# Performance work log

Hardware: AMD Instinct MI355X
Metric: run time of the kernel (lower is better)

## Reference

```python
import jax, jax.numpy as jnp
import numpy as np

N_NODES = 100000
N_EDGES = 1600000  # total after symmetrization (800k pairs + reverses)
N_GRAPHS = 64
D_IN = 64
D_HID = 128
N_CLASSES = 10


def setup_inputs() -> dict:
    key = jax.random.key(0)
    ks = jax.random.split(key, 16)
    half = N_EDGES // 2
    src = jax.random.randint(ks[0], (half,), 0, N_NODES)
    dst = jax.random.randint(ks[1], (half,), 0, N_NODES)
    dst = jnp.where(dst == src, (dst + 1) % N_NODES, dst)  # no self-loops
    # to_undirected: symmetric edge list with fixed shape [2, E]
    edge_index = jnp.stack([jnp.concatenate([src, dst]),
                            jnp.concatenate([dst, src])]).astype(jnp.int64)
    # sorted balanced graph assignment: every graph id present
    batch = ((jnp.arange(N_NODES) * N_GRAPHS) // N_NODES).astype(jnp.int64)

    def lin(k, fi, fo):
        return jax.random.normal(k, (fi, fo), jnp.float32) * (1.0 / np.sqrt(fi))

    inp = {
        'x': jax.random.normal(ks[2], (N_NODES, D_IN), jnp.float32),
        'edge_index': edge_index,
        'batch': batch,
        'gin1_w1': lin(ks[3], D_IN, D_HID), 'gin1_b1': jnp.zeros((D_HID,), jnp.float32),
        'gin1_w2': lin(ks[4], D_HID, D_HID), 'gin1_b2': jnp.zeros((D_HID,), jnp.float32),
        'gin2_w1': lin(ks[5], D_HID, D_HID), 'gin2_b1': jnp.zeros((D_HID,), jnp.float32),
        'gin2_w2': lin(ks[6], D_HID, D_HID), 'gin2_b2': jnp.zeros((D_HID,), jnp.float32),
        'gin3_w1': lin(ks[7], D_HID, D_HID), 'gin3_b1': jnp.zeros((D_HID,), jnp.float32),
        'gin3_w2': lin(ks[8], D_HID, D_HID), 'gin3_b2': jnp.zeros((D_HID,), jnp.float32),
        'fc1_w': lin(ks[9], D_HID, 64), 'fc1_b': jnp.zeros((64,), jnp.float32),
        'fc2_w': lin(ks[10], 64, N_CLASSES), 'fc2_b': jnp.zeros((N_CLASSES,), jnp.float32),
    }
    return inp


def _gin_layer(x, src, dst, w1, b1, w2, b2):
    # GINConv (eps=0): h_i = MLP(x_i + sum_{j in N(i)} x_j)
    agg = jax.ops.segment_sum(x[src], dst, num_segments=N_NODES)
    h = x + agg
    h = jax.nn.relu(h @ w1 + b1)
    return h @ w2 + b2


def reference(x, edge_index, batch,
              gin1_w1, gin1_b1, gin1_w2, gin1_b2,
              gin2_w1, gin2_b1, gin2_w2, gin2_b2,
              gin3_w1, gin3_b1, gin3_w2, gin3_b2,
              fc1_w, fc1_b, fc2_w, fc2_b):
    src, dst = edge_index[0], edge_index[1]
    h = _gin_layer(x, src, dst, gin1_w1, gin1_b1, gin1_w2, gin1_b2)
    h = _gin_layer(h, src, dst, gin2_w1, gin2_b1, gin2_w2, gin2_b2)
    h = _gin_layer(h, src, dst, gin3_w1, gin3_b1, gin3_w2, gin3_b2)
    # global_max_pool over graphs
    pooled = jax.ops.segment_max(h, batch, num_segments=N_GRAPHS)  # [G, D_HID]
    out = jax.nn.relu(pooled @ fc1_w + fc1_b) @ fc2_w + fc2_b
    return jax.nn.log_softmax(out, axis=1)
```

## Files before the change

kernel.cpp:

```cpp
#include <hip/hip_runtime.h>
#include <hip/hip_bf16.h>
#include <cmath>

#define NNODES 100000
#define NGRAPHS 64
#define SHIFT 9
#define NPB 512
#define NB 196
#define CAP 12288
#define BIN_CHUNK 4096
#define HSTRIDE 136
#define CONVBLK 6250

typedef __attribute__((ext_vector_type(8))) short bf16x8;
typedef __attribute__((ext_vector_type(4))) float f32x4;
typedef __attribute__((ext_vector_type(4))) unsigned int u32x4;

__device__ __forceinline__ float bf2f(unsigned short u) {
    unsigned int v = ((unsigned int)u) << 16;
    return __uint_as_float(v);
}
__device__ __forceinline__ unsigned short f2bf(float f) {
    unsigned int v = __float_as_uint(f);
    unsigned int r = (v + 0x7fffu + ((v >> 16) & 1u)) >> 16;
    return (unsigned short)r;
}

__device__ __forceinline__ void atomicMaxF(float* addr, float v) {
    if (v >= 0.f) atomicMax((int*)addr, __float_as_int(v));
    else          atomicMin((unsigned int*)addr, __float_as_uint(v));
}

__device__ __forceinline__ void pack_one(unsigned short* wp, const float* W, int K, int t) {
    int total = (K / 32) * 8 * 64;
    if (t >= total) return;
    int l = t & 63;
    int n0 = (t >> 6) & 7;
    int kp = t >> 9;
    unsigned short o[8];
#pragma unroll
    for (int j = 0; j < 8; ++j)
        o[j] = f2bf(W[(size_t)(kp * 32 + (l >> 4) * 8 + j) * 128 + n0 * 16 + (l & 15)]);
    *(u32x4*)(wp + (size_t)t * 8) = *(u32x4*)o;
}

__global__ __launch_bounds__(256) void setup_kernel(
        unsigned short* __restrict__ B0, const float* __restrict__ x,
        unsigned short* wp1, const float* g1w1,
        unsigned short* wp2, const float* g1w2,
        unsigned short* wp3, const float* g2w1,
        unsigned short* wp4, const float* g2w2,
        unsigned short* wp5, const float* g3w1,
        unsigned short* wp6, const float* g3w2,
        float* __restrict__ pooled, int* __restrict__ gcur) {
    int b = blockIdx.x;
    int t = threadIdx.x;
    if (b < CONVBLK) {
        int i = b * 256 + t;
        float4 v = ((const float4*)x)[i];
        unsigned short o[4] = { f2bf(v.x), f2bf(v.y), f2bf(v.z), f2bf(v.w) };
        ((uint2*)B0)[i] = *(uint2*)o;
        return;
    }
    b -= CONVBLK;
    if (b < 44) {
        if (b < 4)       pack_one(wp1, g1w1, 64,  b * 256 + t);
        else if (b < 12) pack_one(wp2, g1w2, 128, (b - 4) * 256 + t);
        else if (b < 20) pack_one(wp3, g2w1, 128, (b - 12) * 256 + t);
        else if (b < 28) pack_one(wp4, g2w2, 128, (b - 20) * 256 + t);
        else if (b < 36) pack_one(wp5, g3w1, 128, (b - 28) * 256 + t);
        else             pack_one(wp6, g3w2, 128, (b - 36) * 256 + t);
        return;
    }
    b -= 44;
    if (b < 32) {
        pooled[b * 256 + t] = -INFINITY;
        return;
    }
    if (t < NB) gcur[t] = t * CAP;
}

__global__ __launch_bounds__(256) void bin_kernel(unsigned int* __restrict__ binned,
                                                  int* __restrict__ gcur,
                                                  const int* __restrict__ ei, int E) {
    __shared__ int cnt[NB];
    __shared__ int gbase[NB];
    __shared__ int loff[NB];
    int t = threadIdx.x;
    int base = blockIdx.x * BIN_CHUNK;
    for (int i = t; i < NB; i += 256) { cnt[i] = 0; loff[i] = 0; }
    __syncthreads();
    unsigned int pk[16]; short bk[16]; int ne = 0;
#pragma unroll
    for (int i = 0; i < 16; ++i) {
        int e = base + t + i * 256;
        if (e < E) {
            int s = ei[e], d = ei[E + e];
            int b = d >> SHIFT;
            pk[ne] = ((unsigned int)s << SHIFT) | (unsigned int)(d & (NPB - 1));
            bk[ne] = (short)b;
            ne++;
            atomicAdd(&cnt[b], 1);
        }
    }
    __syncthreads();
    for (int i = t; i < NB; i += 256)
        gbase[i] = cnt[i] ? atomicAdd(&gcur[i], cnt[i]) : 0;
    __syncthreads();
    for (int i = 0; i < ne; ++i) {
        int b = bk[i];
        int pos = atomicAdd(&loff[b], 1);
        binned[gbase[b] + pos] = pk[i];
    }
}

__global__ __launch_bounds__(256) void fill2_kernel(int* __restrict__ csr,
                                                    int* __restrict__ start,
                                                    const unsigned int* __restrict__ binned,
                                                    const int* __restrict__ gcur, int N) {
    __shared__ int cur[NPB];
    __shared__ int tsum[256];
    __shared__ int gbs[2];
    int b = blockIdx.x, t = threadIdx.x;
    int n0 = b << SHIFT;
    int nn = N - n0; if (nn > NPB) nn = NPB;
    int c = gcur[b] - b * CAP;
    if (t == 0) {
        int acc = 0, tot = 0;
        for (int i = 0; i < NB; ++i) {
            int ci = gcur[i] - i * CAP;
            if (i < b) acc += ci;
            tot += ci;
        }
        gbs[0] = acc; gbs[1] = tot;
    }
    const unsigned int* eb = binned + (size_t)b * CAP;
    for (int i = t; i < NPB; i += 256) cur[i] = 0;
    __syncthreads();
    int gb = gbs[0];
    for (int p = t; p < c; p += 256) atomicAdd(&cur[eb[p] & (NPB - 1)], 1);
    __syncthreads();
    int v[2]; int s = 0;
#pragma unroll
    for (int i = 0; i < 2; ++i) { v[i] = cur[t * 2 + i]; s += v[i]; }
    int x = s;
    tsum[t] = x;
    __syncthreads();
    for (int off = 1; off < 256; off <<= 1) {
        int y = (t >= off) ? tsum[t - off] : 0;
        __syncthreads();
        x += y;
        tsum[t] = x;
        __syncthreads();
    }
    int run = x - s + gb;
#pragma unroll
    for (int i = 0; i < 2; ++i) {
        int idx = t * 2 + i;
        cur[idx] = run;
        if (idx < nn) start[n0 + idx] = run;
        run += v[i];
    }
    __syncthreads();
    for (int p = t; p < c; p += 256) {
        unsigned int e = eb[p];
        int slot = atomicAdd(&cur[e & (NPB - 1)], 1);
        csr[slot] = (int)(e >> SHIFT);
    }
    if (t == 0 && b == 0) start[N] = gbs[1];
}

template<int K1, bool POOL>
__global__ __launch_bounds__(256) void fused_layer(const unsigned short* __restrict__ Hin,
                                                   const int* __restrict__ start,
                                                   const int* __restrict__ csr,
                                                   const unsigned short* __restrict__ Wp1,
                                                   const float* __restrict__ bias1,
                                                   const unsigned short* __restrict__ Wp2,
                                                   const float* __restrict__ bias2,
                                                   unsigned short* __restrict__ out,
                                                   const int* __restrict__ batch,
                                                   float* __restrict__ pooled, int M) {
    __shared__ unsigned short tile[64 * HSTRIDE];
    __shared__ unsigned int lmax[2][128];
    const int l = threadIdx.x & 63;
    const int w = threadIdx.x >> 6;
    const int rbase = blockIdx.x * 64 + w * 16;
    unsigned short* wt = tile + (w * 16) * HSTRIDE;

    if (POOL) {
        ((unsigned int*)lmax)[threadIdx.x] = 0x007fffffu;
        __syncthreads();
    }

    constexpr int LANES = (K1 == 128) ? 16 : 8;
    constexpr int RPP = 64 / LANES;
    const int rg = l / LANES;
    const int ch = l % LANES;
    const unsigned short* hbb = Hin + ch * 8;
#pragma unroll
    for (int pass = 0; pass < 16 / RPP; ++pass) {
        int rloc = pass * RPP + rg;
        int row = rbase + rloc;
        int rowc = row < M ? row : M - 1;
        float a0[8], a1[8];
        {
            u32x4 v = *(const u32x4*)(hbb + (size_t)rowc * K1);
            const unsigned short* q = (const unsigned short*)&v;
#pragma unroll
            for (int i = 0; i < 8; ++i) { a0[i] = bf2f(q[i]); a1[i] = 0.f; }
        }
        int p0 = start[rowc], p1 = start[rowc + 1];
        int p = p0;
        for (; p + 4 <= p1; p += 4) {
            int j0 = csr[p], j1 = csr[p + 1], j2 = csr[p + 2], j3 = csr[p + 3];
            u32x4 v0 = *(const u32x4*)(hbb + (size_t)j0 * K1);
            u32x4 v1 = *(const u32x4*)(hbb + (size_t)j1 * K1);
            u32x4 v2 = *(const u32x4*)(hbb + (size_t)j2 * K1);
            u32x4 v3 = *(const u32x4*)(hbb + (size_t)j3 * K1);
            const unsigned short* q0 = (const unsigned short*)&v0;
            const unsigned short* q1 = (const unsigned short*)&v1;
            const unsigned short* q2 = (const unsigned short*)&v2;
            const unsigned short* q3 = (const unsigned short*)&v3;
#pragma unroll
            for (int i = 0; i < 8; ++i) a0[i] += bf2f(q0[i]);
#pragma unroll
            for (int i = 0; i < 8; ++i) a1[i] += bf2f(q1[i]);
#pragma unroll
            for (int i = 0; i < 8; ++i) a0[i] += bf2f(q2[i]);
#pragma unroll
            for (int i = 0; i < 8; ++i) a1[i] += bf2f(q3[i]);
        }
        for (; p < p1; ++p) {
            int j = csr[p];
            u32x4 v = *(const u32x4*)(hbb + (size_t)j * K1);
            const unsigned short* q = (const unsigned short*)&v;
#pragma unroll
            for (int i = 0; i < 8; ++i) a0[i] += bf2f(q[i]);
        }
        unsigned short o[8];
#pragma unroll
        for (int i = 0; i < 8; ++i) o[i] = f2bf(a0[i] + a1[i]);
        *(u32x4*)(wt + rloc * HSTRIDE + ch * 8) = *(u32x4*)o;
    }

    const int kgrp = l >> 4;
    const int col = l & 15;
    f32x4 acc[8];
#pragma unroll
    for (int i = 0; i < 8; ++i) acc[i] = (f32x4){0.f, 0.f, 0.f, 0.f};
#pragma unroll
    for (int kp = 0; kp < K1 / 32; ++kp) {
        bf16x8 a = *(const bf16x8*)(wt + col * HSTRIDE + kp * 32 + kgrp * 8);
#pragma unroll
        for (int n0 = 0; n0 < 8; ++n0) {
            bf16x8 bfr = *(const bf16x8*)(Wp1 + ((size_t)(kp * 8 + n0) * 64 + l) * 8);
            acc[n0] = __builtin_amdgcn_mfma_f32_16x16x32_bf16(a, bfr, acc[n0], 0, 0, 0);
        }
    }

#pragma unroll
    for (int n0 = 0; n0 < 8; ++n0) {
        float bv = bias1[n0 * 16 + col];
#pragma unroll
        for (int r = 0; r < 4; ++r) {
            float v = acc[n0][r] + bv;
            v = fmaxf(v, 0.f);
            wt[(kgrp * 4 + r) * HSTRIDE + n0 * 16 + col] = f2bf(v);
        }
    }

    f32x4 acc2[8];
#pragma unroll
    for (int i = 0; i < 8; ++i) acc2[i] = (f32x4){0.f, 0.f, 0.f, 0.f};
#pragma unroll
    for (int kp = 0; kp < 4; ++kp) {
        bf16x8 a2 = *(const bf16x8*)(wt + col * HSTRIDE + kp * 32 + kgrp * 8);
#pragma unroll
        for (int n0 = 0; n0 < 8; ++n0) {
            bf16x8 bfr = *(const bf16x8*)(Wp2 + ((size_t)(kp * 8 + n0) * 64 + l) * 8);
            acc2[n0] = __builtin_amdgcn_mfma_f32_16x16x32_bf16(a2, bfr, acc2[n0], 0, 0, 0);
        }
    }

    const int mbase = rbase;
    if (POOL) {
        int g0 = batch[blockIdx.x * 64];
        int gi[4]; bool ok[4];
#pragma unroll
        for (int r = 0; r < 4; ++r) {
            int row = mbase + kgrp * 4 + r;
            ok[r] = (row < M);
            gi[r] = ok[r] ? (batch[row] - g0) : 0;
        }
#pragma unroll
        for (int n0 = 0; n0 < 8; ++n0) {
            int f = n0 * 16 + col;
            float bv = bias2[f];
#pragma unroll
            for (int r = 0; r < 4; ++r) {
                if (ok[r]) {
                    float v = acc2[n0][r] + bv;
                    unsigned int u = __float_as_uint(v);
                    unsigned int key = (u & 0x80000000u) ? ~u : (u | 0x80000000u);
                    atomicMax(&lmax[gi[r]][f], key);
                }
            }
        }
        __syncthreads();
        int t = threadIdx.x;
        unsigned int key = ((unsigned int*)lmax)[t];
        unsigned int u2 = (key & 0x80000000u) ? (key & 0x7fffffffu) : ~key;
        float v = __uint_as_float(u2);
        int g = g0 + (t >> 7);
        if (g < NGRAPHS && key != 0x007fffffu)
            atomicMaxF(&pooled[g * 128 + (t & 127)], v);
    } else {
#pragma unroll
        for (int n0 = 0; n0 < 8; ++n0) {
            float bv = bias2[n0 * 16 + col];
#pragma unroll
            for (int r = 0; r < 4; ++r) {
                int row = mbase + kgrp * 4 + r;
                if (row < M)
                    out[(size_t)row * 128 + n0 * 16 + col] = f2bf(acc2[n0][r] + bv);
            }
        }
    }
}

__global__ __launch_bounds__(64) void head_kernel(float* __restrict__ out,
                                                  const float* __restrict__ pooled,
                                                  const float* __restrict__ w1,
                                                  const float* __restrict__ b1,
                                                  const float* __restrict__ w2,
                                                  const float* __restrict__ b2) {
    int g = blockIdx.x, t = threadIdx.x;
    __shared__ float a[64];
    __shared__ float o[10];
    __shared__ float red[2];
    const float* pg = pooled + g * 128;
    float acc = b1[t];
    for (int k = 0; k < 128; ++k) acc = fmaf(pg[k], w1[k * 64 + t], acc);
    a[t] = fmaxf(acc, 0.f);
    __syncthreads();
    if (t < 10) {
        float s = b2[t];
        for (int k = 0; k < 64; ++k) s = fmaf(a[k], w2[k * 10 + t], s);
        o[t] = s;
    }
    __syncthreads();
    if (t == 0) {
        float m = -INFINITY;
        for (int c = 0; c < 10; ++c) m = fmaxf(m, o[c]);
        float se = 0.f;
        for (int c = 0; c < 10; ++c) se += expf(o[c] - m);
        red[0] = m;
        red[1] = logf(se);
    }
    __syncthreads();
    if (t < 10) out[g * 10 + t] = o[t] - red[0] - red[1];
}

extern "C" void kernel_launch(void* const* d_in, const int* in_sizes, int n_in,
                              void* d_out, int out_size, void* d_ws, size_t ws_size,
                              hipStream_t stream) {
    const float* x    = (const float*)d_in[0];
    const int* ei     = (const int*)d_in[1];
    const int* batch  = (const int*)d_in[2];
    const float* g1w1 = (const float*)d_in[3];  const float* g1b1 = (const float*)d_in[4];
    const float* g1w2 = (const float*)d_in[5];  const float* g1b2 = (const float*)d_in[6];
    const float* g2w1 = (const float*)d_in[7];  const float* g2b1 = (const float*)d_in[8];
    const float* g2w2 = (const float*)d_in[9];  const float* g2b2 = (const float*)d_in[10];
    const float* g3w1 = (const float*)d_in[11]; const float* g3b1 = (const float*)d_in[12];
    const float* g3w2 = (const float*)d_in[13]; const float* g3b2 = (const float*)d_in[14];
    const float* f1w  = (const float*)d_in[15]; const float* f1b  = (const float*)d_in[16];
    const float* f2w  = (const float*)d_in[17]; const float* f2b  = (const float*)d_in[18];
    float* out = (float*)d_out;

    const int N = NNODES;
    const int E = in_sizes[1] / 2;

    char* base = (char*)d_ws;
    auto alloc = [&](size_t bytes) { char* p = base; base += (bytes + 255) & ~(size_t)255; return p; };

    char* shared_region = alloc((size_t)N * 128 * 2);
    unsigned short* B1 = (unsigned short*)shared_region;
    unsigned int* binned = (unsigned int*)shared_region;
    unsigned short* B2 = (unsigned short*)alloc((size_t)N * 128 * 2);
    unsigned short* B0 = (unsigned short*)alloc((size_t)N * 64 * 2);
    int* csr      = (int*)alloc((size_t)E * 4);
    int* start    = (int*)alloc((size_t)(N + 1) * 4);
    int* gcur     = (int*)alloc((size_t)(NB + 4) * 4);
    float* pooled = (float*)alloc((size_t)NGRAPHS * 128 * 4);
    unsigned short* wp1 = (unsigned short*)alloc((size_t)64 * 128 * 2);
    unsigned short* wp2 = (unsigned short*)alloc((size_t)128 * 128 * 2);
    unsigned short* wp3 = (unsigned short*)alloc((size_t)128 * 128 * 2);
    unsigned short* wp4 = (unsigned short*)alloc((size_t)128 * 128 * 2);
    unsigned short* wp5 = (unsigned short*)alloc((size_t)128 * 128 * 2);
    unsigned short* wp6 = (unsigned short*)alloc((size_t)128 * 128 * 2);

    setup_kernel<<<CONVBLK + 44 + 32 + 1, 256, 0, stream>>>(
        B0, x, wp1, g1w1, wp2, g1w2, wp3, g2w1, wp4, g2w2, wp5, g3w1, wp6, g3w2,
        pooled, gcur);
    bin_kernel<<<(E + BIN_CHUNK - 1) / BIN_CHUNK, 256, 0, stream>>>(binned, gcur, ei, E);
    fill2_kernel<<<NB, 256, 0, stream>>>(csr, start, binned, gcur, N);

    const int pgrid = (N + 63) / 64;

    fused_layer<64, false><<<pgrid, 256, 0, stream>>>(B0, start, csr, wp1, g1b1, wp2, g1b2, B1, batch, pooled, N);
    fused_layer<128, false><<<pgrid, 256, 0, stream>>>(B1, start, csr, wp3, g2b1, wp4, g2b2, B2, batch, pooled, N);
    fused_layer<128, true><<<pgrid, 256, 0, stream>>>(B2, start, csr, wp5, g3b1, wp6, g3b2, (unsigned short*)nullptr, batch, pooled, N);

    head_kernel<<<NGRAPHS, 64, 0, stream>>>(out, pooled, f1w, f1b, f2w, f2b);
}
```

Baseline: 284.3 us.

## Halve rows per block and split MLP output columns across wave pairs

Each block now handles 32 rows instead of 64. Each wave gathers 8 rows. For the two MFMA GEMMs, pairs of waves share a 16-row tile and each wave computes half of the 128 output columns, so per-wave accumulator count and B-fragment loads are halved. Twice as many blocks are launched, and block-wide barriers are added between the gather, GEMM1, ReLU write-back and GEMM2 stages. The aims are more parallelism and occupancy with fewer registers per wave, at the cost of extra __syncthreads and more pooling atomics across the larger grid.

```diff
diff --git a/kernel.cpp b/kernel.cpp
--- a/kernel.cpp
+++ b/kernel.cpp
@@ -181,16 +181,14 @@
                                                    unsigned short* __restrict__ out,
                                                    const int* __restrict__ batch,
                                                    float* __restrict__ pooled, int M) {
-    __shared__ unsigned short tile[64 * HSTRIDE];
+    __shared__ unsigned short tile[32 * HSTRIDE];
     __shared__ unsigned int lmax[2][128];
     const int l = threadIdx.x & 63;
     const int w = threadIdx.x >> 6;
-    const int rbase = blockIdx.x * 64 + w * 16;
-    unsigned short* wt = tile + (w * 16) * HSTRIDE;
+    const int rbase = blockIdx.x * 32;
 
     if (POOL) {
         ((unsigned int*)lmax)[threadIdx.x] = 0x007fffffu;
-        __syncthreads();
     }
 
     constexpr int LANES = (K1 == 128) ? 16 : 8;
@@ -199,8 +197,8 @@
     const int ch = l % LANES;
     const unsigned short* hbb = Hin + ch * 8;
 #pragma unroll
-    for (int pass = 0; pass < 16 / RPP; ++pass) {
-        int rloc = pass * RPP + rg;
+    for (int pass = 0; pass < 8 / RPP; ++pass) {
+        int rloc = w * 8 + pass * RPP + rg;
         int row = rbase + rloc;
         int rowc = row < M ? row : M - 1;
         float a0[8], a1[8];
@@ -241,51 +239,59 @@
         unsigned short o[8];
 #pragma unroll
         for (int i = 0; i < 8; ++i) o[i] = f2bf(a0[i] + a1[i]);
-        *(u32x4*)(wt + rloc * HSTRIDE + ch * 8) = *(u32x4*)o;
-    }
-
+        *(u32x4*)(tile + rloc * HSTRIDE + ch * 8) = *(u32x4*)o;
+    }
+    __syncthreads();
+
+    const int rgrp = w >> 1;
+    const int half = w & 1;
+    unsigned short* wt = tile + (rgrp * 16) * HSTRIDE;
     const int kgrp = l >> 4;
     const int col = l & 15;
-    f32x4 acc[8];
-#pragma unroll
-    for (int i = 0; i < 8; ++i) acc[i] = (f32x4){0.f, 0.f, 0.f, 0.f};
+
+    f32x4 acc[4];
+#pragma unroll
+    for (int i = 0; i < 4; ++i) acc[i] = (f32x4){0.f, 0.f, 0.f, 0.f};
 #pragma unroll
     for (int kp = 0; kp < K1 / 32; ++kp) {
         bf16x8 a = *(const bf16x8*)(wt + col * HSTRIDE + kp * 32 + kgrp * 8);
 #pragma unroll
-        for (int n0 = 0; n0 < 8; ++n0) {
-            bf16x8 bfr = *(const bf16x8*)(Wp1 + ((size_t)(kp * 8 + n0) * 64 + l) * 8);
-            acc[n0] = __builtin_amdgcn_mfma_f32_16x16x32_bf16(a, bfr, acc[n0], 0, 0, 0);
-        }
-    }
-
-#pragma unroll
-    for (int n0 = 0; n0 < 8; ++n0) {
-        float bv = bias1[n0 * 16 + col];
+        for (int n = 0; n < 4; ++n) {
+            bf16x8 bfr = *(const bf16x8*)(Wp1 + ((size_t)(kp * 8 + half * 4 + n) * 64 + l) * 8);
+            acc[n] = __builtin_amdgcn_mfma_f32_16x16x32_bf16(a, bfr, acc[n], 0, 0, 0);
+        }
+    }
+    __syncthreads();
+
+#pragma unroll
+    for (int n = 0; n < 4; ++n) {
+        int f = (half * 4 + n) * 16 + col;
+        float bv = bias1[f];
 #pragma unroll
         for (int r = 0; r < 4; ++r) {
-            float v = acc[n0][r] + bv;
+            float v = acc[n][r] + bv;
             v = fmaxf(v, 0.f);
-            wt[(kgrp * 4 + r) * HSTRIDE + n0 * 16 + col] = f2bf(v);
-        }
-    }
-
-    f32x4 acc2[8];
-#pragma unroll
-    for (int i = 0; i < 8; ++i) acc2[i] = (f32x4){0.f, 0.f, 0.f, 0.f};
+            wt[(kgrp * 4 + r) * HSTRIDE + f] = f2bf(v);
+        }
+    }
+    __syncthreads();
+
+    f32x4 acc2[4];
+#pragma unroll
+    for (int i = 0; i < 4; ++i) acc2[i] = (f32x4){0.f, 0.f, 0.f, 0.f};
 #pragma unroll
     for (int kp = 0; kp < 4; ++kp) {
         bf16x8 a2 = *(const bf16x8*)(wt + col * HSTRIDE + kp * 32 + kgrp * 8);
 #pragma unroll
-        for (int n0 = 0; n0 < 8; ++n0) {
-            bf16x8 bfr = *(const bf16x8*)(Wp2 + ((size_t)(kp * 8 + n0) * 64 + l) * 8);
-            acc2[n0] = __builtin_amdgcn_mfma_f32_16x16x32_bf16(a2, bfr, acc2[n0], 0, 0, 0);
-        }
-    }
-
-    const int mbase = rbase;
+        for (int n = 0; n < 4; ++n) {
+            bf16x8 bfr = *(const bf16x8*)(Wp2 + ((size_t)(kp * 8 + half * 4 + n) * 64 + l) * 8);
+            acc2[n] = __builtin_amdgcn_mfma_f32_16x16x32_bf16(a2, bfr, acc2[n], 0, 0, 0);
+        }
+    }
+
+    const int mbase = rbase + rgrp * 16;
     if (POOL) {
-        int g0 = batch[blockIdx.x * 64];
+        int g0 = batch[rbase];
         int gi[4]; bool ok[4];
 #pragma unroll
         for (int r = 0; r < 4; ++r) {
@@ -294,13 +300,13 @@
             gi[r] = ok[r] ? (batch[row] - g0) : 0;
         }
 #pragma unroll
-        for (int n0 = 0; n0 < 8; ++n0) {
-            int f = n0 * 16 + col;
+        for (int n = 0; n < 4; ++n) {
+            int f = (half * 4 + n) * 16 + col;
             float bv = bias2[f];
 #pragma unroll
             for (int r = 0; r < 4; ++r) {
                 if (ok[r]) {
-                    float v = acc2[n0][r] + bv;
+                    float v = acc2[n][r] + bv;
                     unsigned int u = __float_as_uint(v);
                     unsigned int key = (u & 0x80000000u) ? ~u : (u | 0x80000000u);
                     atomicMax(&lmax[gi[r]][f], key);
@@ -317,13 +323,14 @@
             atomicMaxF(&pooled[g * 128 + (t & 127)], v);
     } else {
 #pragma unroll
-        for (int n0 = 0; n0 < 8; ++n0) {
-            float bv = bias2[n0 * 16 + col];
+        for (int n = 0; n < 4; ++n) {
+            int f = (half * 4 + n) * 16 + col;
+            float bv = bias2[f];
 #pragma unroll
             for (int r = 0; r < 4; ++r) {
                 int row = mbase + kgrp * 4 + r;
                 if (row < M)
-                    out[(size_t)row * 128 + n0 * 16 + col] = f2bf(acc2[n0][r] + bv);
+                    out[(size_t)row * 128 + f] = f2bf(acc2[n][r] + bv);
             }
         }
     }
@@ -406,7 +413,7 @@
     bin_kernel<<<(E + BIN_CHUNK - 1) / BIN_CHUNK, 256, 0, stream>>>(binned, gcur, ei, E);
     fill2_kernel<<<NB, 256, 0, stream>>>(csr, start, binned, gcur, N);
 
-    const int pgrid = (N + 63) / 64;
+    const int pgrid = (N + 31) / 32;
 
     fused_layer<64, false><<<pgrid, 256, 0, stream>>>(B0, start, csr, wp1, g1b1, wp2, g1b2, B1, batch, pooled, N);
     fused_layer<128, false><<<pgrid, 256, 0, stream>>>(B1, start, csr, wp3, g2b1, wp4, g2b2, B2, batch, pooled, N);
```

Result: faster. 268.5 us (-5.5%).
